# Optimization experiments

Measured on AMD Instinct MI355X. Metric: run time of the kernel, lower is better.

## Reference

```python
import jax, jax.numpy as jnp
import numpy as np

MEM = 2048

def _linear_params(key, scale):
    kw, kb = jax.random.split(key)
    W = jax.random.uniform(kw, (MEM, MEM), jnp.float32, -scale, scale)
    b = jax.random.uniform(kb, (MEM,), jnp.float32, -scale, scale)
    return W, b

def setup_inputs() -> dict:
    key = jax.random.key(0)
    ks = jax.random.split(key, 18)
    scale = 1.0 / np.sqrt(MEM)
    inp = {
        'lc': jax.random.normal(ks[0], (1, MEM), jnp.float32),
        'lh': jax.random.normal(ks[1], (1, MEM), jnp.float32),
        'rc': jax.random.normal(ks[2], (1, MEM), jnp.float32),
        'rh': jax.random.normal(ks[3], (1, MEM), jnp.float32),
        'S': jax.random.normal(ks[4], (1, MEM), jnp.float32),
        'w': jax.random.normal(ks[5], (1, MEM), jnp.float32),
    }
    names = ['Wh', 'Us', 'ma', 'ilh', 'irh', 'lflh', 'lfrh', 'rflh', 'rfrh', 'ulh', 'urh']
    for i, n in enumerate(names):
        W, b = _linear_params(ks[6 + i], scale)
        inp[n + '_w'] = W
        inp[n + '_b'] = b
    return inp

def _lin(x, W, b):
    return x @ W.T + b

def reference(lc, lh, rc, rh, S, w,
              Wh_w, Wh_b, Us_w, Us_b, ma_w, ma_b,
              ilh_w, ilh_b, irh_w, irh_b,
              lflh_w, lflh_b, lfrh_w, lfrh_b,
              rflh_w, rflh_b, rfrh_w, rfrh_b,
              ulh_w, ulh_b, urh_w, urh_b):
    # attention scoring over the two children
    m_left = jnp.tanh(_lin(lh, Wh_w, Wh_b) + _lin(S, Us_w, Us_b)).squeeze()   # [MEM]
    m_right = jnp.tanh(_lin(rh, Wh_w, Wh_b) + _lin(S, Us_w, Us_b)).squeeze()  # [MEM]
    exp_left = w @ m_left[:, None]    # [1,1]
    exp_right = w @ m_right[:, None]  # [1,1]
    denom = exp_left + exp_right
    left_alpha = exp_left / denom
    right_alpha = exp_right / denom
    # attention-weighted child hidden states
    la = jnp.tanh(_lin(left_alpha * lh, ma_w, ma_b))   # [1,MEM]
    ra = jnp.tanh(_lin(right_alpha * rh, ma_w, ma_b))  # [1,MEM]
    # tree-LSTM gates
    i = jax.nn.sigmoid(_lin(la, ilh_w, ilh_b) + _lin(ra, irh_w, irh_b))
    lf = jax.nn.sigmoid(_lin(la, lflh_w, lflh_b) + _lin(ra, lfrh_w, lfrh_b))
    rf = jax.nn.sigmoid(_lin(la, rflh_w, rflh_b) + _lin(ra, rfrh_w, rfrh_b))
    update = jnp.tanh(_lin(la, ulh_w, ulh_b) + _lin(ra, urh_w, urh_b))
    c = i * update + lf * lc + rf * rc
    h = jnp.tanh(c)
    return (c, h)
```

## Files before the change

kernel.cpp:

```cpp
#include <hip/hip_runtime.h>
#include <hip/hip_bf16.h>
#include <math.h>

#define MEM 2048
#define NF4 512

__device__ __forceinline__ float dot4(float4 a, float4 b) {
    return a.x * b.x + a.y * b.y + a.z * b.z + a.w * b.w;
}

__device__ __forceinline__ float wave_reduce(float v) {
#pragma unroll
    for (int off = 32; off > 0; off >>= 1)
        v += __shfl_down(v, off, 64);
    return v;
}

__device__ __forceinline__ float sigmoidf_(float x) {
    return 1.0f / (1.0f + expf(-x));
}


__global__ __launch_bounds__(256, 4) void
k1_slab(const float* __restrict__ lh, const float* __restrict__ rh,
        const float* __restrict__ S,
        const float* __restrict__ Wh_w, const float* __restrict__ Us_w,
        const float* __restrict__ ma_w,
        float* __restrict__ ws)
{
    __shared__ __align__(16) float s_x1[MEM];
    __shared__ __align__(16) float s_x2[MEM];

    const int t  = threadIdx.x;
    const int m  = blockIdx.y;
    const int rg = blockIdx.x;

    const float* W  = (m == 0) ? Wh_w : (m == 1) ? Us_w : ma_w;
    const float* x1 = (m == 1) ? S : lh;
    const float* x2 = (m == 1) ? S : rh;

    {
        const float4* a4 = (const float4*)x1;
        const float4* b4 = (const float4*)x2;
        float4* s14 = (float4*)s_x1;
        float4* s24 = (float4*)s_x2;
        for (int i = t; i < NF4; i += 256) { s14[i] = a4[i]; s24[i] = b4[i]; }
    }
    __syncthreads();

    const int wv = t >> 6, ln = t & 63;
    const int row0 = rg * 8 + wv * 2;

    const float4* __restrict__ w0 = (const float4*)(W + (size_t)row0 * MEM);
    const float4* __restrict__ w1 = w0 + NF4;
    const float4* sx1 = (const float4*)s_x1;
    const float4* sx2 = (const float4*)s_x2;

    float4 A[8], B[8];
#pragma unroll
    for (int j = 0; j < 8; ++j) A[j] = w0[j * 64 + ln];
#pragma unroll
    for (int j = 0; j < 8; ++j) B[j] = w1[j * 64 + ln];

    float a00 = 0.f, a01 = 0.f, a10 = 0.f, a11 = 0.f;
#pragma unroll
    for (int j = 0; j < 8; ++j) {
        const float4 p = sx1[j * 64 + ln];
        const float4 q = sx2[j * 64 + ln];
        a00 += dot4(A[j], p); a01 += dot4(A[j], q);
        a10 += dot4(B[j], p); a11 += dot4(B[j], q);
    }
    a00 = wave_reduce(a00); a01 = wave_reduce(a01);
    a10 = wave_reduce(a10); a11 = wave_reduce(a11);

    if (ln == 0) {
        if (m == 0) {
            ws[row0] = a00; ws[row0 + 1] = a10;
            ws[MEM + row0] = a01; ws[MEM + row0 + 1] = a11;
        } else if (m == 1) {
            ws[2 * MEM + row0] = a00; ws[2 * MEM + row0 + 1] = a10;
        } else {
            ws[3 * MEM + row0] = a00; ws[3 * MEM + row0 + 1] = a10;
            ws[4 * MEM + row0] = a01; ws[4 * MEM + row0 + 1] = a11;
        }
    }
}

__global__ __launch_bounds__(1024) void
k_mid(const float* __restrict__ w, const float* __restrict__ Wh_b,
      const float* __restrict__ Us_b, const float* __restrict__ ma_b,
      float* __restrict__ ws)
{
    __shared__ float s_red[16][2];
    __shared__ float s_al[2];

    const int t = threadIdx.x;
    float el = 0.f, er = 0.f;
    for (int j = t; j < MEM; j += 1024) {
        const float us = ws[2 * MEM + j] + Us_b[j];
        const float bb = Wh_b[j] + us;
        const float ml = tanhf(ws[j] + bb);
        const float mr = tanhf(ws[MEM + j] + bb);
        const float wj = w[j];
        el += wj * ml; er += wj * mr;
    }
    el = wave_reduce(el);
    er = wave_reduce(er);
    const int wv = t >> 6, ln = t & 63;
    if (ln == 0) { s_red[wv][0] = el; s_red[wv][1] = er; }
    __syncthreads();
    if (t == 0) {
        float e0 = 0.f, e1 = 0.f;
#pragma unroll
        for (int k = 0; k < 16; ++k) { e0 += s_red[k][0]; e1 += s_red[k][1]; }
        const float d = e0 + e1;
        s_al[0] = e0 / d;
        s_al[1] = e1 / d;
    }
    __syncthreads();
    const float al = s_al[0];
    const float ar = s_al[1];
    for (int j = t; j < MEM; j += 1024) {
        const float mb = ma_b[j];
        const float la = tanhf(al * ws[3 * MEM + j] + mb);
        const float ra = tanhf(ar * ws[4 * MEM + j] + mb);
        ws[j] = la;
        ws[MEM + j] = ra;
    }
}

__global__ __launch_bounds__(256, 4) void
k2_slab(const float* __restrict__ ilh_w,  const float* __restrict__ irh_w,
        const float* __restrict__ lflh_w, const float* __restrict__ lfrh_w,
        const float* __restrict__ rflh_w, const float* __restrict__ rfrh_w,
        const float* __restrict__ ulh_w,  const float* __restrict__ urh_w,
        float* __restrict__ ws)
{
    __shared__ __align__(16) float s_x[MEM];

    const int t  = threadIdx.x;
    const int m  = blockIdx.y;
    const int rg = blockIdx.x;

    const float* Wt[8] = {ilh_w, irh_w, lflh_w, lfrh_w, rflh_w, rfrh_w, ulh_w, urh_w};
    const float* W = Wt[m];
    const float* x = ws + (size_t)(m & 1) * MEM;

    {
        const float4* x4 = (const float4*)x;
        float4* s4 = (float4*)s_x;
        for (int i = t; i < NF4; i += 256) s4[i] = x4[i];
    }
    __syncthreads();

    const int wv = t >> 6, ln = t & 63;
    const int row0 = rg * 8 + wv * 2;

    const float4* __restrict__ w0 = (const float4*)(W + (size_t)row0 * MEM);
    const float4* __restrict__ w1 = w0 + NF4;
    const float4* sx = (const float4*)s_x;

    float4 A[8], B[8];
#pragma unroll
    for (int j = 0; j < 8; ++j) A[j] = w0[j * 64 + ln];
#pragma unroll
    for (int j = 0; j < 8; ++j) B[j] = w1[j * 64 + ln];

    float a0 = 0.f, a1 = 0.f;
#pragma unroll
    for (int j = 0; j < 8; ++j) {
        const float4 xv = sx[j * 64 + ln];
        a0 += dot4(A[j], xv);
        a1 += dot4(B[j], xv);
    }
    a0 = wave_reduce(a0);
    a1 = wave_reduce(a1);
    if (ln == 0) {
        float* p = ws + (size_t)(2 + m) * MEM;
        p[row0]     = a0;
        p[row0 + 1] = a1;
    }
}

__global__ __launch_bounds__(256) void
k3_combine(const float* __restrict__ lc, const float* __restrict__ rc,
           const float* __restrict__ ilh_b,  const float* __restrict__ irh_b,
           const float* __restrict__ lflh_b, const float* __restrict__ lfrh_b,
           const float* __restrict__ rflh_b, const float* __restrict__ rfrh_b,
           const float* __restrict__ ulh_b,  const float* __restrict__ urh_b,
           const float* __restrict__ ws, float* __restrict__ out)
{
    const int j = blockIdx.x * 256 + threadIdx.x;
    const float* P = ws + 2 * MEM;
    const float gi = sigmoidf_(P[j]           + P[MEM + j]     + ilh_b[j]  + irh_b[j]);
    const float lf = sigmoidf_(P[2 * MEM + j] + P[3 * MEM + j] + lflh_b[j] + lfrh_b[j]);
    const float rf = sigmoidf_(P[4 * MEM + j] + P[5 * MEM + j] + rflh_b[j] + rfrh_b[j]);
    const float u  = tanhf(    P[6 * MEM + j] + P[7 * MEM + j] + ulh_b[j]  + urh_b[j]);
    const float c  = gi * u + lf * lc[j] + rf * rc[j];
    out[j]       = c;
    out[MEM + j] = tanhf(c);
}

extern "C" void kernel_launch(void* const* d_in, const int* in_sizes, int n_in,
                              void* d_out, int out_size, void* d_ws, size_t ws_size,
                              hipStream_t stream) {
    const float* lc = (const float*)d_in[0];
    const float* lh = (const float*)d_in[1];
    const float* rc = (const float*)d_in[2];
    const float* rh = (const float*)d_in[3];
    const float* S  = (const float*)d_in[4];
    const float* w  = (const float*)d_in[5];
    const float* Wh_w   = (const float*)d_in[6];   const float* Wh_b   = (const float*)d_in[7];
    const float* Us_w   = (const float*)d_in[8];   const float* Us_b   = (const float*)d_in[9];
    const float* ma_w   = (const float*)d_in[10];  const float* ma_b   = (const float*)d_in[11];
    const float* ilh_w  = (const float*)d_in[12];  const float* ilh_b  = (const float*)d_in[13];
    const float* irh_w  = (const float*)d_in[14];  const float* irh_b  = (const float*)d_in[15];
    const float* lflh_w = (const float*)d_in[16];  const float* lflh_b = (const float*)d_in[17];
    const float* lfrh_w = (const float*)d_in[18];  const float* lfrh_b = (const float*)d_in[19];
    const float* rflh_w = (const float*)d_in[20];  const float* rflh_b = (const float*)d_in[21];
    const float* rfrh_w = (const float*)d_in[22];  const float* rfrh_b = (const float*)d_in[23];
    const float* ulh_w  = (const float*)d_in[24];  const float* ulh_b  = (const float*)d_in[25];
    const float* urh_w  = (const float*)d_in[26];  const float* urh_b  = (const float*)d_in[27];

    float* out = (float*)d_out;
    float* ws  = (float*)d_ws;

    dim3 g1(256, 3);
    k1_slab<<<g1, 256, 0, stream>>>(lh, rh, S, Wh_w, Us_w, ma_w, ws);

    k_mid<<<1, 1024, 0, stream>>>(w, Wh_b, Us_b, ma_b, ws);

    dim3 g2(256, 8);
    k2_slab<<<g2, 256, 0, stream>>>(ilh_w, irh_w, lflh_w, lfrh_w,
                                    rflh_w, rfrh_w, ulh_w, urh_w, ws);

    k3_combine<<<8, 256, 0, stream>>>(lc, rc, ilh_b, irh_b, lflh_b, lfrh_b,
                                      rflh_b, rfrh_b, ulh_b, urh_b, ws, out);
}
```

Measured before the change: 247.2 us.

## Drop LDS staging of input vectors and use smaller 128-thread blocks in GEMV kernels

```diff
diff --git a/kernel.cpp b/kernel.cpp
--- a/kernel.cpp
+++ b/kernel.cpp
@@ -21,54 +21,39 @@
 }
 
 
-__global__ __launch_bounds__(256, 4) void
+__global__ __launch_bounds__(128) void
 k1_slab(const float* __restrict__ lh, const float* __restrict__ rh,
         const float* __restrict__ S,
         const float* __restrict__ Wh_w, const float* __restrict__ Us_w,
         const float* __restrict__ ma_w,
         float* __restrict__ ws)
 {
-    __shared__ __align__(16) float s_x1[MEM];
-    __shared__ __align__(16) float s_x2[MEM];
-
     const int t  = threadIdx.x;
-    const int m  = blockIdx.y;
-    const int rg = blockIdx.x;
+    const int bx = blockIdx.x;
+    const int m  = bx >> 9;
+    const int hs = bx & 511;
+    const int wv = t >> 6, ln = t & 63;
+    const int row0 = hs * 4 + wv * 2;
 
     const float* W  = (m == 0) ? Wh_w : (m == 1) ? Us_w : ma_w;
     const float* x1 = (m == 1) ? S : lh;
     const float* x2 = (m == 1) ? S : rh;
 
-    {
-        const float4* a4 = (const float4*)x1;
-        const float4* b4 = (const float4*)x2;
-        float4* s14 = (float4*)s_x1;
-        float4* s24 = (float4*)s_x2;
-        for (int i = t; i < NF4; i += 256) { s14[i] = a4[i]; s24[i] = b4[i]; }
-    }
-    __syncthreads();
-
-    const int wv = t >> 6, ln = t & 63;
-    const int row0 = rg * 8 + wv * 2;
-
     const float4* __restrict__ w0 = (const float4*)(W + (size_t)row0 * MEM);
     const float4* __restrict__ w1 = w0 + NF4;
-    const float4* sx1 = (const float4*)s_x1;
-    const float4* sx2 = (const float4*)s_x2;
-
-    float4 A[8], B[8];
-#pragma unroll
-    for (int j = 0; j < 8; ++j) A[j] = w0[j * 64 + ln];
-#pragma unroll
-    for (int j = 0; j < 8; ++j) B[j] = w1[j * 64 + ln];
+    const float4* __restrict__ x14 = (const float4*)x1;
+    const float4* __restrict__ x24 = (const float4*)x2;
 
     float a00 = 0.f, a01 = 0.f, a10 = 0.f, a11 = 0.f;
 #pragma unroll
     for (int j = 0; j < 8; ++j) {
-        const float4 p = sx1[j * 64 + ln];
-        const float4 q = sx2[j * 64 + ln];
-        a00 += dot4(A[j], p); a01 += dot4(A[j], q);
-        a10 += dot4(B[j], p); a11 += dot4(B[j], q);
+        const int idx = j * 64 + ln;
+        const float4 A = w0[idx];
+        const float4 B = w1[idx];
+        const float4 p = x14[idx];
+        const float4 q = x24[idx];
+        a00 += dot4(A, p); a01 += dot4(A, q);
+        a10 += dot4(B, p); a11 += dot4(B, q);
     }
     a00 = wave_reduce(a00); a01 = wave_reduce(a01);
     a10 = wave_reduce(a10); a11 = wave_reduce(a11);
@@ -129,49 +114,37 @@
     }
 }
 
-__global__ __launch_bounds__(256, 4) void
+__global__ __launch_bounds__(128) void
 k2_slab(const float* __restrict__ ilh_w,  const float* __restrict__ irh_w,
         const float* __restrict__ lflh_w, const float* __restrict__ lfrh_w,
         const float* __restrict__ rflh_w, const float* __restrict__ rfrh_w,
         const float* __restrict__ ulh_w,  const float* __restrict__ urh_w,
         float* __restrict__ ws)
 {
-    __shared__ __align__(16) float s_x[MEM];
-
     const int t  = threadIdx.x;
-    const int m  = blockIdx.y;
-    const int rg = blockIdx.x;
+    const int bx = blockIdx.x;
+    const int m  = bx >> 9;
+    const int hs = bx & 511;
+    const int wv = t >> 6, ln = t & 63;
+    const int row0 = hs * 4 + wv * 2;
 
     const float* Wt[8] = {ilh_w, irh_w, lflh_w, lfrh_w, rflh_w, rfrh_w, ulh_w, urh_w};
     const float* W = Wt[m];
     const float* x = ws + (size_t)(m & 1) * MEM;
 
-    {
-        const float4* x4 = (const float4*)x;
-        float4* s4 = (float4*)s_x;
-        for (int i = t; i < NF4; i += 256) s4[i] = x4[i];
-    }
-    __syncthreads();
-
-    const int wv = t >> 6, ln = t & 63;
-    const int row0 = rg * 8 + wv * 2;
-
     const float4* __restrict__ w0 = (const float4*)(W + (size_t)row0 * MEM);
     const float4* __restrict__ w1 = w0 + NF4;
-    const float4* sx = (const float4*)s_x;
-
-    float4 A[8], B[8];
-#pragma unroll
-    for (int j = 0; j < 8; ++j) A[j] = w0[j * 64 + ln];
-#pragma unroll
-    for (int j = 0; j < 8; ++j) B[j] = w1[j * 64 + ln];
+    const float4* __restrict__ x4 = (const float4*)x;
 
     float a0 = 0.f, a1 = 0.f;
 #pragma unroll
     for (int j = 0; j < 8; ++j) {
-        const float4 xv = sx[j * 64 + ln];
-        a0 += dot4(A[j], xv);
-        a1 += dot4(B[j], xv);
+        const int idx = j * 64 + ln;
+        const float4 A  = w0[idx];
+        const float4 B  = w1[idx];
+        const float4 xv = x4[idx];
+        a0 += dot4(A, xv);
+        a1 += dot4(B, xv);
     }
     a0 = wave_reduce(a0);
     a1 = wave_reduce(a1);
@@ -225,14 +198,12 @@
     float* out = (float*)d_out;
     float* ws  = (float*)d_ws;
 
-    dim3 g1(256, 3);
-    k1_slab<<<g1, 256, 0, stream>>>(lh, rh, S, Wh_w, Us_w, ma_w, ws);
+    k1_slab<<<1536, 128, 0, stream>>>(lh, rh, S, Wh_w, Us_w, ma_w, ws);
 
     k_mid<<<1, 1024, 0, stream>>>(w, Wh_b, Us_b, ma_b, ws);
 
-    dim3 g2(256, 8);
-    k2_slab<<<g2, 256, 0, stream>>>(ilh_w, irh_w, lflh_w, lfrh_w,
-                                    rflh_w, rfrh_w, ulh_w, urh_w, ws);
+    k2_slab<<<4096, 128, 0, stream>>>(ilh_w, irh_w, lflh_w, lfrh_w,
+                                      rflh_w, rfrh_w, ulh_w, urh_w, ws);
 
     k3_combine<<<8, 256, 0, stream>>>(lc, rc, ilh_b, irh_b, lflh_b, lfrh_b,
                                       rflh_b, rfrh_b, ulh_b, urh_b, ws, out);
```

Result: no change. 247.7 us (+0.2%).
